# Optimization experiments

Hardware: AMD Instinct MI355X
Metric: run time of the kernel (lower is better)

## Reference

```python
import jax, jax.numpy as jnp
import numpy as np

B, N, D = 4, 4096, 512
H = 8
HD = D // H  # 64


def setup_inputs() -> dict:
    key = jax.random.key(0)
    ks = jax.random.split(key, 9)
    s = 1.0 / np.sqrt(D)
    return {
        "x": jax.random.normal(ks[0], (B, N, D), dtype=jnp.float32),
        "Wq": jax.random.normal(ks[1], (D, D), dtype=jnp.float32) * s,
        "bq": jax.random.normal(ks[2], (D,), dtype=jnp.float32) * 0.01,
        "Wk": jax.random.normal(ks[3], (D, D), dtype=jnp.float32) * s,
        "bk": jax.random.normal(ks[4], (D,), dtype=jnp.float32) * 0.01,
        "Wv": jax.random.normal(ks[5], (D, D), dtype=jnp.float32) * s,
        "bv": jax.random.normal(ks[6], (D,), dtype=jnp.float32) * 0.01,
        "Wo": jax.random.normal(ks[7], (D, D), dtype=jnp.float32) * s,
        "bo": jax.random.normal(ks[8], (D,), dtype=jnp.float32) * 0.01,
    }


def reference(x, Wq, bq, Wk, bk, Wv, bv, Wo, bo):
    # projections -> [B, H, N, HD]
    def split_heads(t):
        return t.reshape(B, N, H, HD).transpose(0, 2, 1, 3)

    q = split_heads(x @ Wq.T + bq)
    k = split_heads(x @ Wk.T + bk)
    v = split_heads(x @ Wv.T + bv)

    scale = 1.0 / np.sqrt(HD).astype(np.float32)
    scores = jnp.einsum("bhqd,bhkd->bhqk", q, k) * scale  # [B,H,N,N]
    attn = jax.nn.softmax(scores, axis=-1)
    out = jnp.einsum("bhqk,bhkd->bhqd", attn, v)  # [B,H,N,HD]
    out = out.transpose(0, 2, 1, 3).reshape(B, N, D)
    return out @ Wo.T + bo
```

## Files before the change

### kernel.cpp

```cpp
#include <hip/hip_runtime.h>
#include <hip/hip_bf16.h>

#define BB 4
#define NN 4096
#define DD 512
#define HH 8
#define HD 64

typedef __attribute__((ext_vector_type(4))) float f32x4;
typedef __attribute__((ext_vector_type(16))) float f32x16;
typedef __attribute__((ext_vector_type(8))) short short8;
typedef __attribute__((ext_vector_type(4))) unsigned int uint4v;

static __device__ __forceinline__ unsigned short f2bf(float f) {
    unsigned int u = __float_as_uint(f);
    u += 0x7fff + ((u >> 16) & 1);
    return (unsigned short)(u >> 16);
}

__global__ void convert_bf16(const float* __restrict__ in,
                             unsigned short* __restrict__ out, int n) {
    int i = (blockIdx.x * blockDim.x + threadIdx.x) * 8;
    int stride = gridDim.x * blockDim.x * 8;
    for (; i + 7 < n; i += stride) {
        f32x4 a = *reinterpret_cast<const f32x4*>(in + i);
        f32x4 b = *reinterpret_cast<const f32x4*>(in + i + 4);
        short8 o;
        o[0] = (short)f2bf(a[0]); o[1] = (short)f2bf(a[1]);
        o[2] = (short)f2bf(a[2]); o[3] = (short)f2bf(a[3]);
        o[4] = (short)f2bf(b[0]); o[5] = (short)f2bf(b[1]);
        o[6] = (short)f2bf(b[2]); o[7] = (short)f2bf(b[3]);
        *reinterpret_cast<short8*>(out + i) = o;
    }
}

__global__ void convert_weights(const float* __restrict__ W0, const float* __restrict__ W1,
                                const float* __restrict__ W2, const float* __restrict__ W3,
                                unsigned short* __restrict__ out) {
    int which = blockIdx.x >> 7;
    const float* src = which == 0 ? W0 : which == 1 ? W1 : which == 2 ? W2 : W3;
    unsigned short* dst = out + (size_t)which * DD * DD;
    int i = ((blockIdx.x & 127) * blockDim.x + threadIdx.x) * 8;
    f32x4 a = *reinterpret_cast<const f32x4*>(src + i);
    f32x4 b = *reinterpret_cast<const f32x4*>(src + i + 4);
    short8 o;
    o[0] = (short)f2bf(a[0]); o[1] = (short)f2bf(a[1]);
    o[2] = (short)f2bf(a[2]); o[3] = (short)f2bf(a[3]);
    o[4] = (short)f2bf(b[0]); o[5] = (short)f2bf(b[1]);
    o[6] = (short)f2bf(b[2]); o[7] = (short)f2bf(b[3]);
    *reinterpret_cast<short8*>(dst + i) = o;
}

template <int OUT_BF16>
__device__ __forceinline__
void gemm_tile(const unsigned short* __restrict__ A,
               const unsigned short* __restrict__ W,
               const float* __restrict__ bias,
               void* __restrict__ Cout, float scale,
               int brow, int bcol, uint4* ldsA, uint4* ldsB) {
    const int t = threadIdx.x;
    const int lane = t & 63;
    const int w = t >> 6;
    const int wr = w >> 1, wc = w & 1;
    const int l16 = lane & 15;
    const int lq = lane >> 4;

    f32x4 acc[4][4] = {};

    const int sr = t >> 1;
    const int c16 = (t & 1) * 2;

    for (int k0 = 0; k0 < 512; k0 += 32) {
        const uint4* gA = reinterpret_cast<const uint4*>(A + (size_t)(brow + sr) * 512 + k0 + c16 * 8);
        const uint4* gB = reinterpret_cast<const uint4*>(W + (size_t)(bcol + sr) * 512 + k0 + c16 * 8);
        uint4 a0 = gA[0], a1 = gA[1];
        uint4 b0 = gB[0], b1 = gB[1];
        __syncthreads();
        ldsA[(sr * 4 + c16) ^ (sr & 7)]     = a0;
        ldsA[(sr * 4 + c16 + 1) ^ (sr & 7)] = a1;
        ldsB[(sr * 4 + c16) ^ (sr & 7)]     = b0;
        ldsB[(sr * 4 + c16 + 1) ^ (sr & 7)] = b1;
        __syncthreads();
        short8 af[4], bfr[4];
#pragma unroll
        for (int m = 0; m < 4; ++m) {
            int ra = wr * 64 + m * 16 + l16;
            af[m] = *reinterpret_cast<short8*>(&ldsA[(ra * 4 + lq) ^ (ra & 7)]);
            int rb = wc * 64 + m * 16 + l16;
            bfr[m] = *reinterpret_cast<short8*>(&ldsB[(rb * 4 + lq) ^ (rb & 7)]);
        }
#pragma unroll
        for (int m = 0; m < 4; ++m)
#pragma unroll
            for (int n = 0; n < 4; ++n)
                acc[m][n] = __builtin_amdgcn_mfma_f32_16x16x32_bf16(af[m], bfr[n], acc[m][n], 0, 0, 0);
    }

#pragma unroll
    for (int m = 0; m < 4; ++m) {
        int row = brow + wr * 64 + m * 16 + lq * 4;
#pragma unroll
        for (int n = 0; n < 4; ++n) {
            int col = bcol + wc * 64 + n * 16 + l16;
            float bv = bias[col];
#pragma unroll
            for (int r = 0; r < 4; ++r) {
                float v = (acc[m][n][r] + bv) * scale;
                if (OUT_BF16) {
                    ((unsigned short*)Cout)[(size_t)(row + r) * 512 + col] = f2bf(v);
                } else {
                    ((float*)Cout)[(size_t)(row + r) * 512 + col] = v;
                }
            }
        }
    }
}

__global__ __launch_bounds__(256)
void gemm_qkv(const unsigned short* __restrict__ xb,
              const unsigned short* __restrict__ Wall,
              const float* __restrict__ bq, const float* __restrict__ bk,
              const float* __restrict__ bv,
              unsigned short* __restrict__ Qb, unsigned short* __restrict__ Kb,
              unsigned short* __restrict__ Vb, float cl) {
    __shared__ uint4 ldsA[128 * 4];
    __shared__ uint4 ldsB[128 * 4];
    int z = blockIdx.z;
    const unsigned short* W = Wall + (size_t)z * DD * DD;
    const float* bias = z == 0 ? bq : z == 1 ? bk : bv;
    unsigned short* dst = z == 0 ? Qb : z == 1 ? Kb : Vb;
    float scale = z == 0 ? cl : 1.0f;
    gemm_tile<1>(xb, W, bias, dst, scale,
                 (int)blockIdx.y * 128, (int)blockIdx.x * 128, ldsA, ldsB);
}

__global__ __launch_bounds__(256)
void gemm_bias_f32(const unsigned short* __restrict__ A,
                   const unsigned short* __restrict__ W,
                   const float* __restrict__ bias,
                   float* __restrict__ Cout) {
    __shared__ uint4 ldsA[128 * 4];
    __shared__ uint4 ldsB[128 * 4];
    gemm_tile<0>(A, W, bias, Cout, 1.0f,
                 (int)blockIdx.y * 128, (int)blockIdx.x * 128, ldsA, ldsB);
}

__global__ __launch_bounds__(256)
void transpose_v(const unsigned short* __restrict__ Vb, unsigned short* __restrict__ Vt) {
    __shared__ unsigned short tile[64][72];
    const int bh = blockIdx.y;
    const int b = bh >> 3, h = bh & 7;
    const int n0 = blockIdx.x * 64;
    const int t = threadIdx.x;
    {
        int r = t >> 2;
        int cs = (t & 3) * 16;
        const short8* src = reinterpret_cast<const short8*>(
            Vb + (size_t)(b * NN + n0 + r) * DD + h * HD + cs);
        short8 v0 = src[0], v1 = src[1];
#pragma unroll
        for (int j = 0; j < 8; ++j) {
            tile[r][cs + j]     = (unsigned short)v0[j];
            tile[r][cs + 8 + j] = (unsigned short)v1[j];
        }
    }
    __syncthreads();
    {
        int d = t >> 2;
        int ns = (t & 3) * 16;
        short8 o0, o1;
#pragma unroll
        for (int j = 0; j < 8; ++j) {
            o0[j] = (short)tile[ns + j][d];
            o1[j] = (short)tile[ns + 8 + j][d];
        }
        unsigned short* dst = Vt + ((size_t)bh * HD + d) * NN + n0 + ns;
        *reinterpret_cast<short8*>(dst)     = o0;
        *reinterpret_cast<short8*>(dst + 8) = o1;
    }
}

__global__ __launch_bounds__(256, 3)
void flash_attn(const unsigned short* __restrict__ Qb,
                const unsigned short* __restrict__ Kb,
                const unsigned short* __restrict__ Vt,
                unsigned short* __restrict__ Ob) {
    __shared__ __align__(16) char lds[32768];
    const int t = threadIdx.x;
    const int lane = t & 63;
    const int w = t >> 6;
    const int nid = (blockIdx.x & 7) * 128 + (blockIdx.x >> 3);
    const int bh = nid >> 5;
    const int qb = nid & 31;
    const int b = bh >> 3, h = bh & 7;
    const int q0 = qb * 128 + w * 32;
    const int l32 = lane & 31;
    const int hi = lane >> 5;

    const int i8 = lane >> 3, g8 = lane & 7;

    const unsigned short* qptr = Qb + (size_t)(b * NN + q0 + l32) * DD + h * HD + hi * 8;
    short8 qf[4];
#pragma unroll
    for (int c = 0; c < 4; ++c)
        qf[c] = *reinterpret_cast<const short8*>(qptr + c * 16);

    const f32x16 Z = {};
    f32x16 OT0 = {}, OT1 = {};
    float lsum = 0.f;

    int koff[8], voff[8];
#pragma unroll
    for (int sub = 0; sub < 2; ++sub) {
#pragma unroll
        for (int c = 0; c < 4; ++c) {
            int row = sub * 32 + l32;
            int g = (hi + 2 * c) ^ (row & 7) ^ ((row >> 3) & 7);
            koff[sub * 4 + c] = row * 128 + g * 16;
        }
#pragma unroll
        for (int dblk = 0; dblk < 2; ++dblk)
#pragma unroll
            for (int c2 = 0; c2 < 2; ++c2) {
                int row = dblk * 32 + l32;
                int g = ((sub << 2) + (c2 << 1) + hi) ^ (row & 7) ^ ((row >> 3) & 7);
                voff[sub * 4 + dblk * 2 + c2] = 8192 + row * 128 + g * 16;
            }
    }

    const int rowl0 = w * 16 + i8;
    const int rowl1 = w * 16 + 8 + i8;
    const int gs0 = (g8 ^ i8 ^ ((2 * w) & 7)) * 8;
    const int gs1 = (g8 ^ i8 ^ ((2 * w + 1) & 7)) * 8;
    const unsigned short* kp0 = Kb + (size_t)(b * NN + rowl0) * DD + h * HD + gs0;
    const unsigned short* kp1 = Kb + (size_t)(b * NN + rowl1) * DD + h * HD + gs1;
    const unsigned short* vp0 = Vt + ((size_t)bh * HD + rowl0) * NN + gs0;
    const unsigned short* vp1 = Vt + ((size_t)bh * HD + rowl1) * NN + gs1;

    auto STAGE = [&](int bb) {
        __builtin_amdgcn_global_load_lds(
            (const __attribute__((address_space(1))) void*)kp0,
            (__attribute__((address_space(3))) void*)(lds + bb + (w * 16) * 128), 16, 0, 0);
        __builtin_amdgcn_global_load_lds(
            (const __attribute__((address_space(1))) void*)kp1,
            (__attribute__((address_space(3))) void*)(lds + bb + (w * 16 + 8) * 128), 16, 0, 0);
        __builtin_amdgcn_global_load_lds(
            (const __attribute__((address_space(1))) void*)vp0,
            (__attribute__((address_space(3))) void*)(lds + bb + 8192 + (w * 16) * 128), 16, 0, 0);
        __builtin_amdgcn_global_load_lds(
            (const __attribute__((address_space(1))) void*)vp1,
            (__attribute__((address_space(3))) void*)(lds + bb + 8192 + (w * 16 + 8) * 128), 16, 0, 0);
        kp0 += 64 * DD; kp1 += 64 * DD; vp0 += 64; vp1 += 64;
    };

    auto softpack = [&](const f32x16& S, short8& pa, short8& pb) {
        unsigned int wq[8];
#pragma unroll
        for (int j = 0; j < 8; ++j) {
            float p0 = __builtin_exp2f(S[2 * j]);
            float p1 = __builtin_exp2f(S[2 * j + 1]);
            lsum += p0 + p1;
            asm("v_cvt_pk_bf16_f32 %0, %1, %2" : "=v"(wq[j]) : "v"(p0), "v"(p1));
        }
        asm("v_permlane32_swap_b32 %0, %1" : "+v"(wq[0]), "+v"(wq[2]));
        asm("v_permlane32_swap_b32 %0, %1" : "+v"(wq[1]), "+v"(wq[3]));
        asm("v_permlane32_swap_b32 %0, %1" : "+v"(wq[4]), "+v"(wq[6]));
        asm("v_permlane32_swap_b32 %0, %1" : "+v"(wq[5]), "+v"(wq[7]));
        uint4v pu0 = {wq[0], wq[1], wq[2], wq[3]};
        uint4v pu1 = {wq[4], wq[5], wq[6], wq[7]};
        pa = __builtin_bit_cast(short8, pu0);
        pb = __builtin_bit_cast(short8, pu1);
    };

    auto COMPUTE = [&](int BO) {
#pragma unroll
        for (int sub = 0; sub < 2; ++sub) {
            short8 kf0 = *reinterpret_cast<const short8*>(lds + BO + koff[sub * 4 + 0]);
            short8 kf1 = *reinterpret_cast<const short8*>(lds + BO + koff[sub * 4 + 1]);
            short8 kf2 = *reinterpret_cast<const short8*>(lds + BO + koff[sub * 4 + 2]);
            short8 kf3 = *reinterpret_cast<const short8*>(lds + BO + koff[sub * 4 + 3]);
            f32x16 S;
            S = __builtin_amdgcn_mfma_f32_32x32x16_bf16(kf0, qf[0], Z, 0, 0, 0);
            S = __builtin_amdgcn_mfma_f32_32x32x16_bf16(kf1, qf[1], S, 0, 0, 0);
            S = __builtin_amdgcn_mfma_f32_32x32x16_bf16(kf2, qf[2], S, 0, 0, 0);
            S = __builtin_amdgcn_mfma_f32_32x32x16_bf16(kf3, qf[3], S, 0, 0, 0);
            short8 vf0 = *reinterpret_cast<const short8*>(lds + BO + voff[sub * 4 + 0]);
            short8 vf1 = *reinterpret_cast<const short8*>(lds + BO + voff[sub * 4 + 1]);
            short8 vf2 = *reinterpret_cast<const short8*>(lds + BO + voff[sub * 4 + 2]);
            short8 vf3 = *reinterpret_cast<const short8*>(lds + BO + voff[sub * 4 + 3]);
            short8 pa, pb;
            softpack(S, pa, pb);
            OT0 = __builtin_amdgcn_mfma_f32_32x32x16_bf16(vf0, pa, OT0, 0, 0, 0);
            OT0 = __builtin_amdgcn_mfma_f32_32x32x16_bf16(vf1, pb, OT0, 0, 0, 0);
            OT1 = __builtin_amdgcn_mfma_f32_32x32x16_bf16(vf2, pa, OT1, 0, 0, 0);
            OT1 = __builtin_amdgcn_mfma_f32_32x32x16_bf16(vf3, pb, OT1, 0, 0, 0);
        }
    };

    STAGE(0);
    asm volatile("s_waitcnt vmcnt(0)" ::: "memory");
    __builtin_amdgcn_s_barrier();
    asm volatile("" ::: "memory");

    for (int it = 0; it < 32; ++it) {
        STAGE(16384);
        asm volatile("s_waitcnt vmcnt(4)" ::: "memory");
        __builtin_amdgcn_s_barrier();
        asm volatile("" ::: "memory");
        COMPUTE(0);
        asm volatile("" ::: "memory");
        __builtin_amdgcn_s_barrier();
        asm volatile("" ::: "memory");
        if (it != 31) {
            STAGE(0);
            asm volatile("s_waitcnt vmcnt(4)" ::: "memory");
        } else {
            asm volatile("s_waitcnt vmcnt(0)" ::: "memory");
        }
        __builtin_amdgcn_s_barrier();
        asm volatile("" ::: "memory");
        COMPUTE(16384);
        if (it != 31) {
            asm volatile("" ::: "memory");
            __builtin_amdgcn_s_barrier();
            asm volatile("" ::: "memory");
        }
    }

    lsum += __shfl_xor(lsum, 32);
    float inv = 1.0f / lsum;
    char* lw = lds + w * 4096;
#pragma unroll
    for (int dblk = 0; dblk < 2; ++dblk) {
#pragma unroll
        for (int g = 0; g < 4; ++g) {
#pragma unroll
            for (int j = 0; j < 2; ++j) {
                int r = 4 * g + 2 * j;
                int d = dblk * 32 + 8 * g + 2 * j + 4 * hi;
                float a = (dblk ? OT1[r] : OT0[r]) * inv;
                float bqv = (dblk ? OT1[r + 1] : OT0[r + 1]) * inv;
                unsigned int wv;
                asm("v_cvt_pk_bf16_f32 %0, %1, %2" : "=v"(wv) : "v"(a), "v"(bqv));
                int addr = (l32 * 128 + d * 2) ^ ((l32 & 7) << 4);
                *reinterpret_cast<unsigned int*>(lw + addr) = wv;
            }
        }
    }
#pragma unroll
    for (int it = 0; it < 4; ++it) {
        int q = lane >> 1;
        int seg = (lane & 1) + it * 2;
        uint4 val = *reinterpret_cast<uint4*>(lw + ((q * 128 + seg * 16) ^ ((q & 7) << 4)));
        *reinterpret_cast<uint4*>(Ob + (size_t)(b * NN + q0 + q) * DD + h * HD + seg * 8) = val;
    }
}

extern "C" void kernel_launch(void* const* d_in, const int* in_sizes, int n_in,
                              void* d_out, int out_size, void* d_ws, size_t ws_size,
                              hipStream_t stream) {
    (void)in_sizes; (void)n_in; (void)out_size; (void)ws_size;
    const float* x  = (const float*)d_in[0];
    const float* Wq = (const float*)d_in[1];
    const float* bq = (const float*)d_in[2];
    const float* Wk = (const float*)d_in[3];
    const float* bk = (const float*)d_in[4];
    const float* Wv = (const float*)d_in[5];
    const float* bv = (const float*)d_in[6];
    const float* Wo = (const float*)d_in[7];
    const float* bo = (const float*)d_in[8];
    float* out = (float*)d_out;

    char* ws = (char*)d_ws;
    const size_t BUF = 16777216;
    unsigned short* xb  = (unsigned short*)(ws);
    unsigned short* Qb  = (unsigned short*)(ws + BUF);
    unsigned short* Kb  = (unsigned short*)(ws + 2 * BUF);
    unsigned short* Vb  = (unsigned short*)(ws + 3 * BUF);
    unsigned short* Wqb = (unsigned short*)(ws + 4 * BUF);
    unsigned short* Wob = Wqb + 3 * 262144;
    unsigned short* Vt  = xb;
    unsigned short* Ob  = Vb;

    const int NTOK = BB * NN;
    const float cl = 0.125f * 1.4426950408889634f;

    convert_bf16<<<2048, 256, 0, stream>>>(x, xb, NTOK * DD);
    convert_weights<<<512, 256, 0, stream>>>(Wq, Wk, Wv, Wo, Wqb);

    dim3 ggrid(4, NTOK / 128, 3);
    gemm_qkv<<<ggrid, 256, 0, stream>>>(xb, Wqb, bq, bk, bv, Qb, Kb, Vb, cl);

    transpose_v<<<dim3(NN / 64, BB * HH), 256, 0, stream>>>(Vb, Vt);

    flash_attn<<<1024, 256, 0, stream>>>(Qb, Kb, Vt, Ob);

    gemm_bias_f32<<<dim3(4, NTOK / 128), 256, 0, stream>>>(Ob, Wob, bo, out);
}
```

Measured before the change: 278.5 us.

## Double KV tile to 128 keys per stage with new swizzled LDS layout

Each pipeline stage of the flash-attention kernel now loads 128 keys of K and V instead of 64, so LDS grows to 64KB across two buffers and the loop runs 16 iterations instead of 32. The LDS addressing is reworked around per-lane base offsets XORed by the sub-tile index, and the V tile is laid out with 256-byte rows. This halves the number of barriers and stage handoffs per query block and issues more loads per stage. In exchange, LDS use per block doubles and the occupancy hint of 3 is dropped, which may lower the number of resident blocks per CU.

```diff
diff --git a/kernel.cpp b/kernel.cpp
--- a/kernel.cpp
+++ b/kernel.cpp
@@ -180,12 +180,12 @@
     }
 }
 
-__global__ __launch_bounds__(256, 3)
+__global__ __launch_bounds__(256)
 void flash_attn(const unsigned short* __restrict__ Qb,
                 const unsigned short* __restrict__ Kb,
                 const unsigned short* __restrict__ Vt,
                 unsigned short* __restrict__ Ob) {
-    __shared__ __align__(16) char lds[32768];
+    __shared__ __align__(16) char lds[65536];
     const int t = threadIdx.x;
     const int lane = t & 63;
     const int w = t >> 6;
@@ -196,7 +196,6 @@
     const int q0 = qb * 128 + w * 32;
     const int l32 = lane & 31;
     const int hi = lane >> 5;
-
     const int i8 = lane >> 3, g8 = lane & 7;
 
     const unsigned short* qptr = Qb + (size_t)(b * NN + q0 + l32) * DD + h * HD + hi * 8;
@@ -209,48 +208,42 @@
     f32x16 OT0 = {}, OT1 = {};
     float lsum = 0.f;
 
-    int koff[8], voff[8];
-#pragma unroll
-    for (int sub = 0; sub < 2; ++sub) {
-#pragma unroll
-        for (int c = 0; c < 4; ++c) {
-            int row = sub * 32 + l32;
-            int g = (hi + 2 * c) ^ (row & 7) ^ ((row >> 3) & 7);
-            koff[sub * 4 + c] = row * 128 + g * 16;
-        }
-#pragma unroll
-        for (int dblk = 0; dblk < 2; ++dblk)
-#pragma unroll
-            for (int c2 = 0; c2 < 2; ++c2) {
-                int row = dblk * 32 + l32;
-                int g = ((sub << 2) + (c2 << 1) + hi) ^ (row & 7) ^ ((row >> 3) & 7);
-                voff[sub * 4 + dblk * 2 + c2] = 8192 + row * 128 + g * 16;
-            }
-    }
-
-    const int rowl0 = w * 16 + i8;
-    const int rowl1 = w * 16 + 8 + i8;
-    const int gs0 = (g8 ^ i8 ^ ((2 * w) & 7)) * 8;
-    const int gs1 = (g8 ^ i8 ^ ((2 * w + 1) & 7)) * 8;
-    const unsigned short* kp0 = Kb + (size_t)(b * NN + rowl0) * DD + h * HD + gs0;
-    const unsigned short* kp1 = Kb + (size_t)(b * NN + rowl1) * DD + h * HD + gs1;
-    const unsigned short* vp0 = Vt + ((size_t)bh * HD + rowl0) * NN + gs0;
-    const unsigned short* vp1 = Vt + ((size_t)bh * HD + rowl1) * NN + gs1;
+    int kbase[4];
+#pragma unroll
+    for (int c = 0; c < 4; ++c)
+        kbase[c] = l32 * 128 + (((2 * c + hi) ^ (l32 & 7) ^ (l32 >> 3)) << 4);
+    int vbase[2];
+#pragma unroll
+    for (int c2 = 0; c2 < 2; ++c2)
+        vbase[c2] = l32 * 256 + (((2 * c2 + hi) ^ (l32 & 7) ^ (l32 >> 3)) << 4);
+
+    const unsigned short* kp[4];
+    const unsigned short* vp[4];
+#pragma unroll
+    for (int jj = 0; jj < 4; ++jj) {
+        int rl = w * 32 + jj * 8 + i8;
+        int gk = g8 ^ i8 ^ ((w * 4 + jj) & 7);
+        kp[jj] = Kb + (size_t)(b * NN + rl) * DD + h * HD + gk * 8;
+        int dv = w * 16 + jj * 4 + (lane >> 4);
+        int gv = (lane & 15) ^ (dv & 7) ^ ((dv >> 3) & 7);
+        vp[jj] = Vt + ((size_t)bh * HD + dv) * NN + gv * 8;
+    }
 
     auto STAGE = [&](int bb) {
-        __builtin_amdgcn_global_load_lds(
-            (const __attribute__((address_space(1))) void*)kp0,
-            (__attribute__((address_space(3))) void*)(lds + bb + (w * 16) * 128), 16, 0, 0);
-        __builtin_amdgcn_global_load_lds(
-            (const __attribute__((address_space(1))) void*)kp1,
-            (__attribute__((address_space(3))) void*)(lds + bb + (w * 16 + 8) * 128), 16, 0, 0);
-        __builtin_amdgcn_global_load_lds(
-            (const __attribute__((address_space(1))) void*)vp0,
-            (__attribute__((address_space(3))) void*)(lds + bb + 8192 + (w * 16) * 128), 16, 0, 0);
-        __builtin_amdgcn_global_load_lds(
-            (const __attribute__((address_space(1))) void*)vp1,
-            (__attribute__((address_space(3))) void*)(lds + bb + 8192 + (w * 16 + 8) * 128), 16, 0, 0);
-        kp0 += 64 * DD; kp1 += 64 * DD; vp0 += 64; vp1 += 64;
+#pragma unroll
+        for (int jj = 0; jj < 4; ++jj) {
+            __builtin_amdgcn_global_load_lds(
+                (const __attribute__((address_space(1))) void*)kp[jj],
+                (__attribute__((address_space(3))) void*)(lds + bb + (w * 32 + jj * 8) * 128), 16, 0, 0);
+            kp[jj] += 128 * DD;
+        }
+#pragma unroll
+        for (int jj = 0; jj < 4; ++jj) {
+            __builtin_amdgcn_global_load_lds(
+                (const __attribute__((address_space(1))) void*)vp[jj],
+                (__attribute__((address_space(3))) void*)(lds + bb + 16384 + (w * 4 + jj) * 1024), 16, 0, 0);
+            vp[jj] += 128;
+        }
     };
 
     auto softpack = [&](const f32x16& S, short8& pa, short8& pb) {
@@ -274,20 +267,23 @@
 
     auto COMPUTE = [&](int BO) {
 #pragma unroll
-        for (int sub = 0; sub < 2; ++sub) {
-            short8 kf0 = *reinterpret_cast<const short8*>(lds + BO + koff[sub * 4 + 0]);
-            short8 kf1 = *reinterpret_cast<const short8*>(lds + BO + koff[sub * 4 + 1]);
-            short8 kf2 = *reinterpret_cast<const short8*>(lds + BO + koff[sub * 4 + 2]);
-            short8 kf3 = *reinterpret_cast<const short8*>(lds + BO + koff[sub * 4 + 3]);
+        for (int sub = 0; sub < 4; ++sub) {
+            const int kx = (sub & 1) << 6;
+            short8 kf0 = *reinterpret_cast<const short8*>(lds + BO + sub * 4096 + (kbase[0] ^ kx));
+            short8 kf1 = *reinterpret_cast<const short8*>(lds + BO + sub * 4096 + (kbase[1] ^ kx));
+            short8 kf2 = *reinterpret_cast<const short8*>(lds + BO + sub * 4096 + (kbase[2] ^ kx));
+            short8 kf3 = *reinterpret_cast<const short8*>(lds + BO + sub * 4096 + (kbase[3] ^ kx));
             f32x16 S;
             S = __builtin_amdgcn_mfma_f32_32x32x16_bf16(kf0, qf[0], Z, 0, 0, 0);
             S = __builtin_amdgcn_mfma_f32_32x32x16_bf16(kf1, qf[1], S, 0, 0, 0);
             S = __builtin_amdgcn_mfma_f32_32x32x16_bf16(kf2, qf[2], S, 0, 0, 0);
             S = __builtin_amdgcn_mfma_f32_32x32x16_bf16(kf3, qf[3], S, 0, 0, 0);
-            short8 vf0 = *reinterpret_cast<const short8*>(lds + BO + voff[sub * 4 + 0]);
-            short8 vf1 = *reinterpret_cast<const short8*>(lds + BO + voff[sub * 4 + 1]);
-            short8 vf2 = *reinterpret_cast<const short8*>(lds + BO + voff[sub * 4 + 2]);
-            short8 vf3 = *reinterpret_cast<const short8*>(lds + BO + voff[sub * 4 + 3]);
+            const int vx0 = ((sub ^ 0) & 3) << 6;
+            const int vx1 = ((sub ^ 1) & 3) << 6;
+            short8 vf0 = *reinterpret_cast<const short8*>(lds + BO + 16384 +        (vbase[0] ^ vx0));
+            short8 vf1 = *reinterpret_cast<const short8*>(lds + BO + 16384 +        (vbase[1] ^ vx0));
+            short8 vf2 = *reinterpret_cast<const short8*>(lds + BO + 16384 + 8192 + (vbase[0] ^ vx1));
+            short8 vf3 = *reinterpret_cast<const short8*>(lds + BO + 16384 + 8192 + (vbase[1] ^ vx1));
             short8 pa, pb;
             softpack(S, pa, pb);
             OT0 = __builtin_amdgcn_mfma_f32_32x32x16_bf16(vf0, pa, OT0, 0, 0, 0);
@@ -298,29 +294,26 @@
     };
 
     STAGE(0);
-    asm volatile("s_waitcnt vmcnt(0)" ::: "memory");
-    __builtin_amdgcn_s_barrier();
-    asm volatile("" ::: "memory");
-
-    for (int it = 0; it < 32; ++it) {
-        STAGE(16384);
-        asm volatile("s_waitcnt vmcnt(4)" ::: "memory");
+
+    for (int it = 0; it < 16; ++it) {
+        STAGE(32768);
+        asm volatile("s_waitcnt vmcnt(8)" ::: "memory");
         __builtin_amdgcn_s_barrier();
         asm volatile("" ::: "memory");
         COMPUTE(0);
         asm volatile("" ::: "memory");
         __builtin_amdgcn_s_barrier();
         asm volatile("" ::: "memory");
-        if (it != 31) {
+        if (it != 15) {
             STAGE(0);
-            asm volatile("s_waitcnt vmcnt(4)" ::: "memory");
+            asm volatile("s_waitcnt vmcnt(8)" ::: "memory");
         } else {
             asm volatile("s_waitcnt vmcnt(0)" ::: "memory");
         }
         __builtin_amdgcn_s_barrier();
         asm volatile("" ::: "memory");
-        COMPUTE(16384);
-        if (it != 31) {
+        COMPUTE(32768);
+        if (it != 15) {
             asm volatile("" ::: "memory");
             __builtin_amdgcn_s_barrier();
             asm volatile("" ::: "memory");
```

Result: slower. 342.6 us (+23.0%).

## Fuse V transpose into QKV GEMM epilogue and halve flash-attn block size

Applied to the files above, without the earlier changes.

The V projection epilogue now writes bf16 directly in the transposed [B*H, HD, N] layout, so the separate transpose_v kernel and its extra round trip through global memory go away. The flash attention kernel moves from 4 to 2 waves per block with 64 query rows, doubling the grid to 2048 blocks. Each wave now stages 4 K and 4 V rows per tile, and the vmcnt waits are raised to match. The trade-offs are less reuse of each K/V tile in LDS, different occupancy because the min-blocks launch bound was dropped, and more scattered transposed stores in the GEMM epilogue.

```diff
diff --git a/kernel.cpp b/kernel.cpp
--- a/kernel.cpp
+++ b/kernel.cpp
@@ -51,7 +51,7 @@
     *reinterpret_cast<short8*>(dst + i) = o;
 }
 
-template <int OUT_BF16>
+template <int OUT_MODE>
 __device__ __forceinline__
 void gemm_tile(const unsigned short* __restrict__ A,
                const unsigned short* __restrict__ W,
@@ -103,13 +103,26 @@
         for (int n = 0; n < 4; ++n) {
             int col = bcol + wc * 64 + n * 16 + l16;
             float bv = bias[col];
-#pragma unroll
-            for (int r = 0; r < 4; ++r) {
-                float v = (acc[m][n][r] + bv) * scale;
-                if (OUT_BF16) {
-                    ((unsigned short*)Cout)[(size_t)(row + r) * 512 + col] = f2bf(v);
-                } else {
-                    ((float*)Cout)[(size_t)(row + r) * 512 + col] = v;
+            if (OUT_MODE == 2) {
+                int bh = ((row >> 12) << 3) + (col >> 6);
+                int d = col & 63;
+                int ntok = row & 4095;
+                ushort4 o;
+                o.x = f2bf(acc[m][n][0] + bv);
+                o.y = f2bf(acc[m][n][1] + bv);
+                o.z = f2bf(acc[m][n][2] + bv);
+                o.w = f2bf(acc[m][n][3] + bv);
+                *reinterpret_cast<ushort4*>(
+                    (unsigned short*)Cout + ((size_t)bh * 64 + d) * 4096 + ntok) = o;
+            } else {
+#pragma unroll
+                for (int r = 0; r < 4; ++r) {
+                    float v = (acc[m][n][r] + bv) * scale;
+                    if (OUT_MODE == 1) {
+                        ((unsigned short*)Cout)[(size_t)(row + r) * 512 + col] = f2bf(v);
+                    } else {
+                        ((float*)Cout)[(size_t)(row + r) * 512 + col] = v;
+                    }
                 }
             }
         }
@@ -122,16 +135,19 @@
               const float* __restrict__ bq, const float* __restrict__ bk,
               const float* __restrict__ bv,
               unsigned short* __restrict__ Qb, unsigned short* __restrict__ Kb,
-              unsigned short* __restrict__ Vb, float cl) {
+              unsigned short* __restrict__ Vt, float cl) {
     __shared__ uint4 ldsA[128 * 4];
     __shared__ uint4 ldsB[128 * 4];
     int z = blockIdx.z;
     const unsigned short* W = Wall + (size_t)z * DD * DD;
-    const float* bias = z == 0 ? bq : z == 1 ? bk : bv;
-    unsigned short* dst = z == 0 ? Qb : z == 1 ? Kb : Vb;
-    float scale = z == 0 ? cl : 1.0f;
-    gemm_tile<1>(xb, W, bias, dst, scale,
-                 (int)blockIdx.y * 128, (int)blockIdx.x * 128, ldsA, ldsB);
+    int brow = (int)blockIdx.y * 128, bcol = (int)blockIdx.x * 128;
+    if (z == 0) {
+        gemm_tile<1>(xb, W, bq, Qb, cl, brow, bcol, ldsA, ldsB);
+    } else if (z == 1) {
+        gemm_tile<1>(xb, W, bk, Kb, 1.0f, brow, bcol, ldsA, ldsB);
+    } else {
+        gemm_tile<2>(xb, W, bv, Vt, 1.0f, brow, bcol, ldsA, ldsB);
+    }
 }
 
 __global__ __launch_bounds__(256)
@@ -145,42 +161,7 @@
                  (int)blockIdx.y * 128, (int)blockIdx.x * 128, ldsA, ldsB);
 }
 
-__global__ __launch_bounds__(256)
-void transpose_v(const unsigned short* __restrict__ Vb, unsigned short* __restrict__ Vt) {
-    __shared__ unsigned short tile[64][72];
-    const int bh = blockIdx.y;
-    const int b = bh >> 3, h = bh & 7;
-    const int n0 = blockIdx.x * 64;
-    const int t = threadIdx.x;
-    {
-        int r = t >> 2;
-        int cs = (t & 3) * 16;
-        const short8* src = reinterpret_cast<const short8*>(
-            Vb + (size_t)(b * NN + n0 + r) * DD + h * HD + cs);
-        short8 v0 = src[0], v1 = src[1];
-#pragma unroll
-        for (int j = 0; j < 8; ++j) {
-            tile[r][cs + j]     = (unsigned short)v0[j];
-            tile[r][cs + 8 + j] = (unsigned short)v1[j];
-        }
-    }
-    __syncthreads();
-    {
-        int d = t >> 2;
-        int ns = (t & 3) * 16;
-        short8 o0, o1;
-#pragma unroll
-        for (int j = 0; j < 8; ++j) {
-            o0[j] = (short)tile[ns + j][d];
-            o1[j] = (short)tile[ns + 8 + j][d];
-        }
-        unsigned short* dst = Vt + ((size_t)bh * HD + d) * NN + n0 + ns;
-        *reinterpret_cast<short8*>(dst)     = o0;
-        *reinterpret_cast<short8*>(dst + 8) = o1;
-    }
-}
-
-__global__ __launch_bounds__(256, 3)
+__global__ __launch_bounds__(128)
 void flash_attn(const unsigned short* __restrict__ Qb,
                 const unsigned short* __restrict__ Kb,
                 const unsigned short* __restrict__ Vt,
@@ -189,11 +170,11 @@
     const int t = threadIdx.x;
     const int lane = t & 63;
     const int w = t >> 6;
-    const int nid = (blockIdx.x & 7) * 128 + (blockIdx.x >> 3);
-    const int bh = nid >> 5;
-    const int qb = nid & 31;
+    const int nid = (blockIdx.x & 7) * 256 + (blockIdx.x >> 3);
+    const int bh = nid >> 6;
+    const int qb = nid & 63;
     const int b = bh >> 3, h = bh & 7;
-    const int q0 = qb * 128 + w * 32;
+    const int q0 = qb * 64 + w * 32;
     const int l32 = lane & 31;
     const int hi = lane >> 5;
 
@@ -228,29 +209,31 @@
             }
     }
 
-    const int rowl0 = w * 16 + i8;
-    const int rowl1 = w * 16 + 8 + i8;
-    const int gs0 = (g8 ^ i8 ^ ((2 * w) & 7)) * 8;
-    const int gs1 = (g8 ^ i8 ^ ((2 * w + 1) & 7)) * 8;
-    const unsigned short* kp0 = Kb + (size_t)(b * NN + rowl0) * DD + h * HD + gs0;
-    const unsigned short* kp1 = Kb + (size_t)(b * NN + rowl1) * DD + h * HD + gs1;
-    const unsigned short* vp0 = Vt + ((size_t)bh * HD + rowl0) * NN + gs0;
-    const unsigned short* vp1 = Vt + ((size_t)bh * HD + rowl1) * NN + gs1;
+    const unsigned short* kp[4];
+    const unsigned short* vp[4];
+#pragma unroll
+    for (int jj = 0; jj < 4; ++jj) {
+        int rl = w * 32 + jj * 8 + i8;
+        int gk = (g8 ^ i8 ^ ((w * 4 + jj) & 7)) * 8;
+        kp[jj] = Kb + (size_t)(b * NN + rl) * DD + h * HD + gk;
+        vp[jj] = Vt + ((size_t)bh * HD + rl) * NN + gk;
+    }
 
     auto STAGE = [&](int bb) {
-        __builtin_amdgcn_global_load_lds(
-            (const __attribute__((address_space(1))) void*)kp0,
-            (__attribute__((address_space(3))) void*)(lds + bb + (w * 16) * 128), 16, 0, 0);
-        __builtin_amdgcn_global_load_lds(
-            (const __attribute__((address_space(1))) void*)kp1,
-            (__attribute__((address_space(3))) void*)(lds + bb + (w * 16 + 8) * 128), 16, 0, 0);
-        __builtin_amdgcn_global_load_lds(
-            (const __attribute__((address_space(1))) void*)vp0,
-            (__attribute__((address_space(3))) void*)(lds + bb + 8192 + (w * 16) * 128), 16, 0, 0);
-        __builtin_amdgcn_global_load_lds(
-            (const __attribute__((address_space(1))) void*)vp1,
-            (__attribute__((address_space(3))) void*)(lds + bb + 8192 + (w * 16 + 8) * 128), 16, 0, 0);
-        kp0 += 64 * DD; kp1 += 64 * DD; vp0 += 64; vp1 += 64;
+#pragma unroll
+        for (int jj = 0; jj < 4; ++jj) {
+            __builtin_amdgcn_global_load_lds(
+                (const __attribute__((address_space(1))) void*)kp[jj],
+                (__attribute__((address_space(3))) void*)(lds + bb + (w * 32 + jj * 8) * 128), 16, 0, 0);
+            kp[jj] += 64 * DD;
+        }
+#pragma unroll
+        for (int jj = 0; jj < 4; ++jj) {
+            __builtin_amdgcn_global_load_lds(
+                (const __attribute__((address_space(1))) void*)vp[jj],
+                (__attribute__((address_space(3))) void*)(lds + bb + 8192 + (w * 32 + jj * 8) * 128), 16, 0, 0);
+            vp[jj] += 64;
+        }
     };
 
     auto softpack = [&](const f32x16& S, short8& pa, short8& pb) {
@@ -304,7 +287,7 @@
 
     for (int it = 0; it < 32; ++it) {
         STAGE(16384);
-        asm volatile("s_waitcnt vmcnt(4)" ::: "memory");
+        asm volatile("s_waitcnt vmcnt(8)" ::: "memory");
         __builtin_amdgcn_s_barrier();
         asm volatile("" ::: "memory");
         COMPUTE(0);
@@ -313,7 +296,7 @@
         asm volatile("" ::: "memory");
         if (it != 31) {
             STAGE(0);
-            asm volatile("s_waitcnt vmcnt(4)" ::: "memory");
+            asm volatile("s_waitcnt vmcnt(8)" ::: "memory");
         } else {
             asm volatile("s_waitcnt vmcnt(0)" ::: "memory");
         }
@@ -376,11 +359,10 @@
     unsigned short* xb  = (unsigned short*)(ws);
     unsigned short* Qb  = (unsigned short*)(ws + BUF);
     unsigned short* Kb  = (unsigned short*)(ws + 2 * BUF);
-    unsigned short* Vb  = (unsigned short*)(ws + 3 * BUF);
+    unsigned short* Vt  = (unsigned short*)(ws + 3 * BUF);
     unsigned short* Wqb = (unsigned short*)(ws + 4 * BUF);
     unsigned short* Wob = Wqb + 3 * 262144;
-    unsigned short* Vt  = xb;
-    unsigned short* Ob  = Vb;
+    unsigned short* Ob  = xb;
 
     const int NTOK = BB * NN;
     const float cl = 0.125f * 1.4426950408889634f;
@@ -389,11 +371,9 @@
     convert_weights<<<512, 256, 0, stream>>>(Wq, Wk, Wv, Wo, Wqb);
 
     dim3 ggrid(4, NTOK / 128, 3);
-    gemm_qkv<<<ggrid, 256, 0, stream>>>(xb, Wqb, bq, bk, bv, Qb, Kb, Vb, cl);
-
-    transpose_v<<<dim3(NN / 64, BB * HH), 256, 0, stream>>>(Vb, Vt);
-
-    flash_attn<<<1024, 256, 0, stream>>>(Qb, Kb, Vt, Ob);
+    gemm_qkv<<<ggrid, 256, 0, stream>>>(xb, Wqb, bq, bk, bv, Qb, Kb, Vt, cl);
+
+    flash_attn<<<2048, 128, 0, stream>>>(Qb, Kb, Vt, Ob);
 
     gemm_bias_f32<<<dim3(4, NTOK / 128), 256, 0, stream>>>(Ob, Wob, bo, out);
 }
```

Result: slower. 322.0 us (+15.6%).
